# Kernel tuning notes

Measured on AMD Instinct MI355X. Metric: run time of the kernel, lower is better.

## Reference

```python
import jax, jax.numpy as jnp
import numpy as np

B, T, D, D_OUT = 8, 2048, 1024, 1024


def setup_inputs() -> dict:
    key = jax.random.key(0)
    k1, k2 = jax.random.split(key)
    x = jax.random.normal(k1, (B, T, D), dtype=jnp.float32)
    # dense projection params (Linear(D, D_OUT)); scaled init for stability
    W = jax.random.normal(k2, (D, D_OUT), dtype=jnp.float32) / np.sqrt(D)
    b = jnp.zeros((D_OUT,), dtype=jnp.float32)
    return {"x": x, "W": W, "b": b}


def reference(x, W, b):
    # x_: [B, T, D_OUT] projected tensor (self.dense(x))
    x_ = jnp.einsum("btd,de->bte", x, W) + b
    # correlation_matrix: [B, T, T], scaled by sqrt(d_out)
    scores = jnp.einsum("bte,bse->bts", x_, x_) / jnp.sqrt(jnp.asarray(D_OUT, x.dtype))
    # additive causal mask: -inf above the diagonal (triu, diagonal=1)
    causal = jnp.triu(jnp.full((T, T), -jnp.inf, dtype=x.dtype), k=1)
    scores = scores + causal
    # NOTE: original uses nn.Softmax(1) -> softmax over dim 1 (columns), not -1
    attn = jax.nn.softmax(scores, axis=1)
    # V is the RAW input x, not the projected x_
    return jnp.einsum("bts,bsd->btd", attn, x)
```

## Files before the change

kernel.cpp:

```cpp
#include <hip/hip_runtime.h>
#include <hip/hip_bf16.h>


#define B_ 8
#define T_ 2048
#define D_ 1024
#define E_ 1024
#define PIT 56

typedef unsigned short u16;
typedef __attribute__((ext_vector_type(8))) short short8;
typedef __attribute__((ext_vector_type(4))) float floatx4;

__device__ __forceinline__ float b2f(u16 u) {
    unsigned v = ((unsigned)u) << 16;
    float f; __builtin_memcpy(&f, &v, 4); return f;
}
__device__ __forceinline__ u16 f2b(float f) {
    unsigned v; __builtin_memcpy(&v, &f, 4);
    v = (v + 0x7FFFu + ((v >> 16) & 1u)) >> 16;
    return (u16)v;
}
__device__ __forceinline__ unsigned pkbf(float a, float b) {
    __hip_bfloat162 h = __float22bfloat162_rn(make_float2(a, b));
    unsigned u; __builtin_memcpy(&u, &h, 4); return u;
}

__device__ __forceinline__ void gl2lds16(const u16* gp, u16* lp) {
    __builtin_amdgcn_global_load_lds(
        (const __attribute__((address_space(1))) void*)(gp),
        (__attribute__((address_space(3))) void*)(lp), 16, 0, 0);
}

__device__ __forceinline__ void stage8(const u16* src, size_t srow, int kc,
                                       u16* lds, int wid, int lane)
{
    const int rl = lane >> 3, c = lane & 7;
    const int g = ((c ^ rl) << 3);
#pragma unroll
    for (int cc = 0; cc < 2; cc++) {
        const int r = cc * 64 + wid * 8;
        gl2lds16(src + (size_t)(r + rl) * srow + kc + g, &lds[r * 64]);
    }
}

__device__ __forceinline__ void gemm_step(const u16* As_, const u16* Bs_,
                                          int wr, int wc, int l15, int q, int sw,
                                          floatx4 (&acc)[2][4])
{
#pragma unroll
    for (int h = 0; h < 2; h++) {
        short8 a[2], b2[4];
#pragma unroll
        for (int i = 0; i < 2; i++)
            a[i] = *(const short8*)&As_[(wr + i * 16 + l15) * 64 + (((h * 4 + q) ^ sw) << 3)];
#pragma unroll
        for (int j = 0; j < 4; j++)
            b2[j] = *(const short8*)&Bs_[(wc + j * 16 + l15) * 64 + (((h * 4 + q) ^ sw) << 3)];
#pragma unroll
        for (int i = 0; i < 2; i++)
#pragma unroll
            for (int j = 0; j < 4; j++)
                acc[i][j] = __builtin_amdgcn_mfma_f32_16x16x32_bf16(a[i], b2[j], acc[i][j], 0, 0, 0);
    }
}

__device__ __forceinline__ float* mr_ptr(u16* S, int which, int b, int s) {
    const int row = which * 32 + b * 4 + (s >> 9);
    return (float*)(S + (size_t)row * T_ + 1024 + (s & 511) * 2);
}
__device__ __forceinline__ float2* part2_ptr(u16* S, int it, int b, int s) {
    const int row = 64 + it * 8 + (s >> 8);
    return (float2*)(S + (size_t)b * T_ * T_ + (size_t)row * T_ + 1024 + (s & 255) * 4);
}

__global__ __launch_bounds__(256) void k0_wt(const float* __restrict__ W,
                                             u16* __restrict__ WT)
{
    __shared__ float Ws[64 * 68];
    const int tid = threadIdx.x;
    const int k0 = blockIdx.x * 64, n0 = blockIdx.y * 64;
#pragma unroll
    for (int u = 0; u < 4; u++) {
        const int c = tid + 256 * u;
        const int row = c >> 4, c4 = c & 15;
        float4 v = *(const float4*)(W + (size_t)(k0 + row) * E_ + n0 + c4 * 4);
        *(float4*)&Ws[row * 68 + c4 * 4] = v;
    }
    __syncthreads();
#pragma unroll
    for (int u = 0; u < 2; u++) {
        const int c = tid + 256 * u;
        const int n = c >> 3, kc = c & 7;
        unsigned pk[4];
#pragma unroll
        for (int j = 0; j < 4; j++)
            pk[j] = pkbf(Ws[(kc * 8 + 2 * j) * 68 + n], Ws[(kc * 8 + 2 * j + 1) * 68 + n]);
        *(uint4*)(WT + (size_t)(n0 + n) * D_ + k0 + kc * 8) = make_uint4(pk[0], pk[1], pk[2], pk[3]);
    }
}

__global__ __launch_bounds__(256) void k00_xt(const float* __restrict__ x,
                                              u16* __restrict__ XT,
                                              u16* __restrict__ xbf,
                                              int do_xt)
{
    __shared__ float Xs[64 * 68];
    const int tid = threadIdx.x;
    const int s0 = blockIdx.x * 64, d0 = blockIdx.y * 64, b = blockIdx.z;
    const float* xb = x + (size_t)b * T_ * D_;
#pragma unroll
    for (int u = 0; u < 4; u++) {
        const int c = tid + 256 * u;
        const int row = c >> 4, c4 = c & 15;
        float4 v = *(const float4*)(xb + (size_t)(s0 + row) * D_ + d0 + c4 * 4);
        *(float4*)&Xs[row * 68 + c4 * 4] = v;
    }
    __syncthreads();
#pragma unroll
    for (int u = 0; u < 2; u++) {
        const int c = tid + 256 * u;
        const int row = c >> 3, off = c & 7;
        unsigned pk[4];
#pragma unroll
        for (int j = 0; j < 4; j++)
            pk[j] = pkbf(Xs[row * 68 + off * 8 + 2 * j], Xs[row * 68 + off * 8 + 2 * j + 1]);
        *(uint4*)(xbf + ((size_t)(b * T_ + s0 + row)) * D_ + d0 + off * 8) =
            make_uint4(pk[0], pk[1], pk[2], pk[3]);
    }
    if (!do_xt) return;
#pragma unroll
    for (int u = 0; u < 2; u++) {
        const int c = tid + 256 * u;
        const int d = c >> 3, sc = c & 7;
        unsigned pk[4];
#pragma unroll
        for (int j = 0; j < 4; j++)
            pk[j] = pkbf(Xs[(sc * 8 + 2 * j) * 68 + d], Xs[(sc * 8 + 2 * j + 1) * 68 + d]);
        *(uint4*)(XT + ((size_t)(b * D_ + d0 + d)) * T_ + s0 + sc * 8) =
            make_uint4(pk[0], pk[1], pk[2], pk[3]);
    }
}

__global__ __launch_bounds__(512, 4) void k1_proj(const u16* __restrict__ xbf,
                                                  const u16* __restrict__ WT,
                                                  const float* __restrict__ bias,
                                                  u16* __restrict__ y)
{
    __shared__ u16 As[2][128 * 64];
    __shared__ u16 Bs[2][128 * 64];
    const int tid = threadIdx.x;
    const int lane = tid & 63, wid = tid >> 6;
    const int wr = (wid >> 1) * 32, wc = (wid & 1) * 64;
    const int l15 = lane & 15, q = lane >> 4;
    const int sw = l15 & 7;
    const int lin = blockIdx.y * 8 + blockIdx.x;
    const int v = (lin & 7) * 128 + (lin >> 3);
    const int n0 = (v & 7) * 128, m0 = (v >> 3) * 128;
    const u16* Ab = xbf + (size_t)m0 * D_;
    const u16* Bb = WT + (size_t)n0 * D_;

    floatx4 acc[2][4];
#pragma unroll
    for (int i = 0; i < 2; i++)
#pragma unroll
        for (int j = 0; j < 4; j++) acc[i][j] = (floatx4){0.f, 0.f, 0.f, 0.f};

    stage8(Ab, D_, 0, As[0], wid, lane);
    stage8(Bb, D_, 0, Bs[0], wid, lane);
    __syncthreads();
    int cur = 0;
    for (int t = 0; t < 16; t++) {
        if (t + 1 < 16) {
            stage8(Ab, D_, (t + 1) * 64, As[cur ^ 1], wid, lane);
            stage8(Bb, D_, (t + 1) * 64, Bs[cur ^ 1], wid, lane);
        }
        gemm_step(As[cur], Bs[cur], wr, wc, l15, q, sw, acc);
        __syncthreads();
        cur ^= 1;
    }
    float bv[4];
#pragma unroll
    for (int j = 0; j < 4; j++) bv[j] = bias[n0 + wc + j * 16 + l15];
#pragma unroll
    for (int i = 0; i < 2; i++)
#pragma unroll
        for (int j = 0; j < 4; j++)
#pragma unroll
            for (int r = 0; r < 4; r++) {
                const int gm = m0 + wr + i * 16 + q * 4 + r;
                const int gn = n0 + wc + j * 16 + l15;
                y[(size_t)gm * E_ + gn] = f2b(acc[i][j][r] + bv[j]);
            }
}

__global__ __launch_bounds__(512, 4) void k2_score(const u16* __restrict__ y,
                                                   u16* __restrict__ S)
{
    __shared__ u16 As[2][128 * 64];
    __shared__ u16 Bs[2][128 * 64];
    __shared__ float smf[8][64], smz[8][64];
    const int tid = threadIdx.x;
    const int lane = tid & 63, wid = tid >> 6;
    const int wr = (wid >> 1) * 32, wc = (wid & 1) * 64;
    const int l15 = lane & 15, q = lane >> 4;
    const int sw = l15 & 7;
    const int lin = blockIdx.x;
    const int b = lin & 7;
    int idx = lin >> 3;
    int it = 0, base = 0;
    while (base + it + 1 <= idx) { base += it + 1; it++; }
    const int js = idx - base;
    const int t0 = it * 128, s0 = js * 128;
    const u16* yb = y + (size_t)b * T_ * E_;
    const u16* Ab = yb + (size_t)t0 * E_;
    const u16* Bb = yb + (size_t)s0 * E_;

    floatx4 acc[2][4];
#pragma unroll
    for (int i = 0; i < 2; i++)
#pragma unroll
        for (int j = 0; j < 4; j++) acc[i][j] = (floatx4){0.f, 0.f, 0.f, 0.f};

    stage8(Ab, E_, 0, As[0], wid, lane);
    stage8(Bb, E_, 0, Bs[0], wid, lane);
    __syncthreads();
    int cur = 0;
    for (int t = 0; t < 16; t++) {
        if (t + 1 < 16) {
            stage8(Ab, E_, (t + 1) * 64, As[cur ^ 1], wid, lane);
            stage8(Bb, E_, (t + 1) * 64, Bs[cur ^ 1], wid, lane);
        }
        gemm_step(As[cur], Bs[cur], wr, wc, l15, q, sw, acc);
        __syncthreads();
        cur ^= 1;
    }
    float pm[4] = {-1e38f, -1e38f, -1e38f, -1e38f};
    float pz[4] = {0.f, 0.f, 0.f, 0.f};
    u16 ov[2][4][4];
#pragma unroll
    for (int i = 0; i < 2; i++)
#pragma unroll
        for (int j = 0; j < 4; j++)
#pragma unroll
            for (int r = 0; r < 4; r++) {
                const int t = t0 + wr + i * 16 + q * 4 + r;
                const int s = s0 + wc + j * 16 + l15;
                u16 o = (t < s) ? (u16)0xFF7F : f2b(acc[i][j][r] * 0.03125f);
                S[((size_t)(b * T_ + t)) * T_ + s] = o;
                ov[i][j][r] = o;
                if (t >= s) pm[j] = fmaxf(pm[j], b2f(o));
            }
#pragma unroll
    for (int i = 0; i < 2; i++)
#pragma unroll
        for (int j = 0; j < 4; j++)
#pragma unroll
            for (int r = 0; r < 4; r++) {
                const int t = t0 + wr + i * 16 + q * 4 + r;
                const int s = s0 + wc + j * 16 + l15;
                const float ez = __expf(b2f(ov[i][j][r]) - pm[j]);
                pz[j] += (t >= s) ? ez : 0.f;
            }
#pragma unroll
    for (int j = 0; j < 4; j++) {
#pragma unroll
        for (int d = 16; d < 64; d <<= 1) {
            const float om = __shfl_xor(pm[j], d);
            const float oz = __shfl_xor(pz[j], d);
            const float nm = fmaxf(pm[j], om);
            pz[j] = pz[j] * __expf(pm[j] - nm) + oz * __expf(om - nm);
            pm[j] = nm;
        }
    }
    if (q == 0)
#pragma unroll
        for (int j = 0; j < 4; j++) {
            smf[wid][j * 16 + l15] = pm[j];
            smz[wid][j * 16 + l15] = pz[j];
        }
    __syncthreads();
    if (tid < 128) {
        const int half = tid >> 6, cidx = tid & 63;
        float M = -1e38f, Z = 0.f;
#pragma unroll
        for (int g = 0; g < 4; g++) {
            const float m2 = smf[g * 2 + half][cidx];
            const float z2 = smz[g * 2 + half][cidx];
            const float nm = fmaxf(M, m2);
            Z = Z * __expf(M - nm) + z2 * __expf(m2 - nm);
            M = nm;
        }
        *part2_ptr(S, it, b, s0 + half * 64 + cidx) = make_float2(M, Z);
    }
}

__global__ __launch_bounds__(256) void k2c_comb(u16* __restrict__ S)
{
    const int s = blockIdx.x * 256 + threadIdx.x;
    const int b = blockIdx.y;
    float M = -1e38f, Z = 0.f;
    for (int it = s >> 7; it < 16; it++) {
        const float2 p = *part2_ptr(S, it, b, s);
        const float nm = fmaxf(M, p.x);
        Z = Z * __expf(M - nm) + p.y * __expf(p.x - nm);
        M = nm;
    }
    *mr_ptr(S, 0, b, s) = M;
    *mr_ptr(S, 1, b, s) = 1.0f / Z;
}

__global__ __launch_bounds__(256) void k3_pnorm(u16* __restrict__ S)
{
    const int row = blockIdx.x;
    const int b = row >> 11;
    const int t = row & (T_ - 1);
    const int sEnd = ((t >> 7) + 1) << 7;
    const int s0 = threadIdx.x * 8;
    if (s0 >= sEnd) return;
    u16* Sp = S + (size_t)row * T_ + s0;
    const float* mp = mr_ptr(S, 0, b, s0);
    const float* rp = mr_ptr(S, 1, b, s0);
    float mv[8], rv[8];
    *(float4*)&mv[0] = *(const float4*)mp;
    *(float4*)&mv[4] = *((const float4*)mp + 1);
    *(float4*)&rv[0] = *(const float4*)rp;
    *(float4*)&rv[4] = *((const float4*)rp + 1);
    ushort4 v0 = *(ushort4*)Sp;
    ushort4 v1 = *(ushort4*)(Sp + 4);
    u16 vv[8] = { v0.x, v0.y, v0.z, v0.w, v1.x, v1.y, v1.z, v1.w };
    u16 ov[8];
#pragma unroll
    for (int i = 0; i < 8; i++) {
        const int s = s0 + i;
        float p = 0.f;
        if (s <= t) p = __expf(b2f(vv[i]) - mv[i]) * rv[i];
        ov[i] = f2b(p);
    }
    *(ushort4*)Sp       = make_ushort4(ov[0], ov[1], ov[2], ov[3]);
    *(ushort4*)(Sp + 4) = make_ushort4(ov[4], ov[5], ov[6], ov[7]);
}

__global__ __launch_bounds__(512, 4) void k4_fast(const u16* __restrict__ P,
                                                  const u16* __restrict__ XT,
                                                  float* __restrict__ out)
{
    __shared__ u16 As[2][128 * 64];
    __shared__ u16 Bs[2][128 * 64];
    const int tid = threadIdx.x;
    const int lane = tid & 63, wid = tid >> 6;
    const int wr = (wid >> 1) * 32, wc = (wid & 1) * 64;
    const int l15 = lane & 15, q = lane >> 4;
    const int sw = l15 & 7;
    const int lin = blockIdx.x;
    const int b = lin & 7;
    const int r8 = lin >> 3;
    const int d0 = (r8 & 7) * 128;
    const int it = (T_ / 128 - 1) - (r8 >> 3);
    const int t0 = it * 128;
    const u16* Pb = P + (size_t)b * T_ * T_ + (size_t)t0 * T_;
    const u16* Xb = XT + (size_t)(b * D_ + d0) * T_;

    floatx4 acc[2][4];
#pragma unroll
    for (int i = 0; i < 2; i++)
#pragma unroll
        for (int j = 0; j < 4; j++) acc[i][j] = (floatx4){0.f, 0.f, 0.f, 0.f};

    const int nt = (it + 1) * 2;
    stage8(Pb, T_, 0, As[0], wid, lane);
    stage8(Xb, T_, 0, Bs[0], wid, lane);
    __syncthreads();
    int cur = 0;
    for (int t = 0; t < nt; t++) {
        if (t + 1 < nt) {
            stage8(Pb, T_, (t + 1) * 64, As[cur ^ 1], wid, lane);
            stage8(Xb, T_, (t + 1) * 64, Bs[cur ^ 1], wid, lane);
        }
        gemm_step(As[cur], Bs[cur], wr, wc, l15, q, sw, acc);
        __syncthreads();
        cur ^= 1;
    }
#pragma unroll
    for (int i = 0; i < 2; i++)
#pragma unroll
        for (int j = 0; j < 4; j++)
#pragma unroll
            for (int r = 0; r < 4; r++) {
                const int gt = t0 + wr + i * 16 + q * 4 + r;
                const int gd = d0 + wc + j * 16 + l15;
                out[(size_t)(b * T_ + gt) * D_ + gd] = acc[i][j][r];
            }
}

__global__ __launch_bounds__(256) void k4_fb(const u16* __restrict__ P,
                                             const float* __restrict__ x,
                                             float* __restrict__ out)
{
    __shared__ u16 As[128 * PIT];
    __shared__ u16 Bs[128 * PIT];
    const int tid = threadIdx.x;
    const int lane = tid & 63, wid = tid >> 6;
    const int wr = (wid >> 1) * 64, wc = (wid & 1) * 64;
    const int l15 = lane & 15, q = lane >> 4;
    const int it = (T_ / 128 - 1) - blockIdx.y;
    const int t0 = it * 128;
    const int d0 = blockIdx.x * 128;
    const int b = blockIdx.z;
    const u16* Pb = P + (size_t)b * T_ * T_;
    const float* xb = x + (size_t)b * T_ * D_;
    const int gn = tid & 127;
    const int kh0 = (tid >> 7) * 2;

    floatx4 acc[4][4];
#pragma unroll
    for (int i = 0; i < 4; i++)
#pragma unroll
        for (int j = 0; j < 4; j++) acc[i][j] = (floatx4){0.f, 0.f, 0.f, 0.f};

    const int kend = t0 + 128;
    for (int k0 = 0; k0 < kend; k0 += 32) {
        __syncthreads();
#pragma unroll
        for (int u = 0; u < 2; u++) {
            const int c = tid * 2 + u;
            const int row = c >> 2, off = c & 3;
            *(uint4*)&As[row * PIT + off * 8] =
                *(const uint4*)(Pb + (size_t)(t0 + row) * T_ + k0 + off * 8);
        }
#pragma unroll
        for (int u = 0; u < 2; u++) {
            const int kh = kh0 + u;
            float f[8];
#pragma unroll
            for (int j = 0; j < 8; j++)
                f[j] = xb[(size_t)(k0 + kh * 8 + j) * D_ + d0 + gn];
            uint4 pk = make_uint4(pkbf(f[0], f[1]), pkbf(f[2], f[3]),
                                  pkbf(f[4], f[5]), pkbf(f[6], f[7]));
            *(uint4*)&Bs[gn * PIT + kh * 8] = pk;
        }
        __syncthreads();
        short8 a[4], b2[4];
#pragma unroll
        for (int i = 0; i < 4; i++) a[i] = *(const short8*)&As[(wr + i * 16 + l15) * PIT + q * 8];
#pragma unroll
        for (int j = 0; j < 4; j++) b2[j] = *(const short8*)&Bs[(wc + j * 16 + l15) * PIT + q * 8];
#pragma unroll
        for (int i = 0; i < 4; i++)
#pragma unroll
            for (int j = 0; j < 4; j++)
                acc[i][j] = __builtin_amdgcn_mfma_f32_16x16x32_bf16(a[i], b2[j], acc[i][j], 0, 0, 0);
    }
#pragma unroll
    for (int i = 0; i < 4; i++)
#pragma unroll
        for (int j = 0; j < 4; j++)
#pragma unroll
            for (int r = 0; r < 4; r++) {
                const int gt = t0 + wr + i * 16 + q * 4 + r;
                const int gd = d0 + wc + j * 16 + l15;
                out[(size_t)(b * T_ + gt) * D_ + gd] = acc[i][j][r];
            }
}

extern "C" void kernel_launch(void* const* d_in, const int* in_sizes, int n_in,
                              void* d_out, int out_size, void* d_ws, size_t ws_size,
                              hipStream_t stream)
{
    const float* x    = (const float*)d_in[0];
    const float* W    = (const float*)d_in[1];
    const float* bias = (const float*)d_in[2];
    float* outf = (float*)d_out;
    u16*   y    = (u16*)d_out;
    u16*   WT   = y + ((size_t)1 << 24);
    u16*   S    = (u16*)d_ws;
    u16*   xbf  = S;
    u16*   XT   = S + ((size_t)1 << 25);
    const bool fast = ws_size >= ((size_t)96 << 20);

    dim3 g0(D_ / 64, E_ / 64);
    k0_wt<<<g0, 256, 0, stream>>>(W, WT);

    dim3 g00(T_ / 64, D_ / 64, B_);
    k00_xt<<<g00, 256, 0, stream>>>(x, XT, xbf, fast ? 1 : 0);

    dim3 g1(E_ / 128, (B_ * T_) / 128);
    k1_proj<<<g1, 512, 0, stream>>>(xbf, WT, bias, y);

    dim3 g2(136 * B_);
    k2_score<<<g2, 512, 0, stream>>>(y, S);

    dim3 gc(T_ / 256, B_);
    k2c_comb<<<gc, 256, 0, stream>>>(S);

    dim3 g3(B_ * T_);
    k3_pnorm<<<g3, 256, 0, stream>>>(S);

    dim3 g4((D_ / 128) * (T_ / 128) * B_);
    if (fast) k4_fast<<<g4, 512, 0, stream>>>(S, XT, outf);
    else {
        dim3 g4b(D_ / 128, T_ / 128, B_);
        k4_fb<<<g4b, 256, 0, stream>>>(S, x, outf);
    }
}
```

Before: 291.6 us.

## Fuse column-stat combine into tile-wise normalization over lower-triangular tiles only

In the fast path, the separate column max/sum combine kernel and the per-row normalization kernel are replaced by one kernel launched over only the 136 lower-triangular 128x128 tiles per batch. Each block recombines the partial column statistics it needs and normalizes its own tile in place, applying the causal zeroing on diagonal tiles. This removes a launch and avoids reading and writing the fully masked upper-triangular region. The cost is that every tile recomputes the statistic combine redundantly. The score kernel also keeps float values in registers instead of re-expanding stored bf16.

```diff
diff --git a/kernel.cpp b/kernel.cpp
--- a/kernel.cpp
+++ b/kernel.cpp
@@ -235,9 +235,9 @@
         __syncthreads();
         cur ^= 1;
     }
+    float fv[2][4][4];
     float pm[4] = {-1e38f, -1e38f, -1e38f, -1e38f};
     float pz[4] = {0.f, 0.f, 0.f, 0.f};
-    u16 ov[2][4][4];
 #pragma unroll
     for (int i = 0; i < 2; i++)
 #pragma unroll
@@ -248,8 +248,9 @@
                 const int s = s0 + wc + j * 16 + l15;
                 u16 o = (t < s) ? (u16)0xFF7F : f2b(acc[i][j][r] * 0.03125f);
                 S[((size_t)(b * T_ + t)) * T_ + s] = o;
-                ov[i][j][r] = o;
-                if (t >= s) pm[j] = fmaxf(pm[j], b2f(o));
+                const float fo = b2f(o);
+                fv[i][j][r] = fo;
+                if (t >= s) pm[j] = fmaxf(pm[j], fo);
             }
 #pragma unroll
     for (int i = 0; i < 2; i++)
@@ -259,7 +260,7 @@
             for (int r = 0; r < 4; r++) {
                 const int t = t0 + wr + i * 16 + q * 4 + r;
                 const int s = s0 + wc + j * 16 + l15;
-                const float ez = __expf(b2f(ov[i][j][r]) - pm[j]);
+                const float ez = __expf(fv[i][j][r] - pm[j]);
                 pz[j] += (t >= s) ? ez : 0.f;
             }
 #pragma unroll
@@ -292,6 +293,57 @@
             M = nm;
         }
         *part2_ptr(S, it, b, s0 + half * 64 + cidx) = make_float2(M, Z);
+    }
+}
+
+__global__ __launch_bounds__(256) void k3_tile(u16* __restrict__ S)
+{
+    __shared__ float lm[128], lr[128];
+    const int tid = threadIdx.x;
+    const int lin = blockIdx.x;
+    const int b = lin & 7;
+    int idx = lin >> 3, it = 0, base = 0;
+    while (base + it + 1 <= idx) { base += it + 1; it++; }
+    const int js = idx - base;
+    const int t0 = it * 128, s0 = js * 128;
+    if (tid < 128) {
+        const int s = s0 + tid;
+        float M = -1e38f, Z = 0.f;
+        for (int i2 = js; i2 < 16; i2++) {
+            const float2 p = *part2_ptr(S, i2, b, s);
+            const float nm = fmaxf(M, p.x);
+            Z = Z * __expf(M - nm) + p.y * __expf(p.x - nm);
+            M = nm;
+        }
+        lm[tid] = M;
+        lr[tid] = 1.0f / Z;
+    }
+    __syncthreads();
+    u16* Sb = S + (size_t)b * T_ * T_;
+    const int c8 = (tid & 15) * 8;
+    const int r0 = tid >> 4;
+    float mv[8], rv[8];
+    *(float4*)&mv[0] = *(const float4*)&lm[c8];
+    *(float4*)&mv[4] = *(const float4*)&lm[c8 + 4];
+    *(float4*)&rv[0] = *(const float4*)&lr[c8];
+    *(float4*)&rv[4] = *(const float4*)&lr[c8 + 4];
+    const bool diag = (it == js);
+#pragma unroll
+    for (int rr = 0; rr < 8; rr++) {
+        const int t = t0 + r0 + rr * 16;
+        u16* Sp = Sb + (size_t)t * T_ + s0 + c8;
+        ushort4 v0 = *(ushort4*)Sp;
+        ushort4 v1 = *(ushort4*)(Sp + 4);
+        u16 vv[8] = { v0.x, v0.y, v0.z, v0.w, v1.x, v1.y, v1.z, v1.w };
+        u16 ov[8];
+#pragma unroll
+        for (int i = 0; i < 8; i++) {
+            float p = __expf(b2f(vv[i]) - mv[i]) * rv[i];
+            if (diag && (s0 + c8 + i > t)) p = 0.f;
+            ov[i] = f2b(p);
+        }
+        *(ushort4*)Sp       = make_ushort4(ov[0], ov[1], ov[2], ov[3]);
+        *(ushort4*)(Sp + 4) = make_ushort4(ov[4], ov[5], ov[6], ov[7]);
     }
 }
 
@@ -490,15 +542,16 @@
     dim3 g2(136 * B_);
     k2_score<<<g2, 512, 0, stream>>>(y, S);
 
-    dim3 gc(T_ / 256, B_);
-    k2c_comb<<<gc, 256, 0, stream>>>(S);
-
-    dim3 g3(B_ * T_);
-    k3_pnorm<<<g3, 256, 0, stream>>>(S);
-
     dim3 g4((D_ / 128) * (T_ / 128) * B_);
-    if (fast) k4_fast<<<g4, 512, 0, stream>>>(S, XT, outf);
-    else {
+    if (fast) {
+        dim3 g3t(136 * B_);
+        k3_tile<<<g3t, 256, 0, stream>>>(S);
+        k4_fast<<<g4, 512, 0, stream>>>(S, XT, outf);
+    } else {
+        dim3 gc(T_ / 256, B_);
+        k2c_comb<<<gc, 256, 0, stream>>>(S);
+        dim3 g3(B_ * T_);
+        k3_pnorm<<<g3, 256, 0, stream>>>(S);
         dim3 g4b(D_ / 128, T_ / 128, B_);
         k4_fb<<<g4b, 256, 0, stream>>>(S, x, outf);
     }
```

New measurement: 277.8 us. -4.7%, faster.
